# Kernel optimization log

Measured on AMD Instinct MI355X. Metric: run time of the kernel, lower is better.

Reference implementation:

```python
import jax, jax.numpy as jnp
import numpy as np

EPS = 1e-7
NORM_EPS = 1e-12

def _l2norm(x, axis):
    n = jnp.sqrt(jnp.sum(x * x, axis=axis, keepdims=True))
    return x / jnp.maximum(n, NORM_EPS)

def setup_inputs() -> dict:
    key = jax.random.key(0)
    B, M, D, N = 8, 64, 256, 16384
    ks = jax.random.split(key, 10)
    inp = {
        "points": jax.random.normal(ks[0], (B, D, N), jnp.float32),
        "clusters": jax.random.normal(ks[1], (B, M, D), jnp.float32),
        "values": jax.random.normal(ks[2], (B, N, D), jnp.float32),
        "value_clusters": jax.random.normal(ks[3], (B, M, D), jnp.float32),
        # learned params
        "sim_alpha": jnp.ones((M,), jnp.float32),
        "sim_beta": jnp.zeros((M,), jnp.float32),
        "clusters_bias": jnp.zeros((M, D), jnp.float32),
        "Wc": jax.random.normal(ks[4], (D, D), jnp.float32) / np.sqrt(D),
        "bc": jnp.zeros((D,), jnp.float32),
        "value_clusters_bias": jnp.zeros((M, D), jnp.float32),
        "Wv": jax.random.normal(ks[5], (D, D), jnp.float32) / np.sqrt(D),
        "bv": jnp.zeros((D,), jnp.float32),
    }
    return inp

def reference(points, clusters, values, value_clusters,
              sim_alpha, sim_beta, clusters_bias, Wc, bc,
              value_clusters_bias, Wv, bv):
    # per-cluster bias + Linear + SiLU (with_cluster_bias=True, no position)
    c = jax.nn.silu((clusters + clusters_bias) @ Wc.T + bc)            # [B,M,D]
    vc = jax.nn.silu((value_clusters + value_clusters_bias) @ Wv.T + bv)  # [B,M,D]
    # cosine similarity: normalize clusters over last dim, points over dim=-2
    sim = _l2norm(c, -1) @ _l2norm(points, -2)                         # [B,M,N]
    sim = sim_alpha[None, :, None] * sim + sim_beta[None, :, None]
    assignment = jax.nn.softmax(sim, axis=1)                           # over clusters
    agg = (vc + assignment @ values) / (jnp.sum(assignment, axis=-1, keepdims=True) + EPS)  # [B,M,D]
    # x = agg^T @ assignment -> [B,D,N]
    x = jnp.einsum('bmd,bmn->bdn', agg, assignment)
    return x
```

## Files before the change

kernel.cpp:

```cpp
#include <hip/hip_runtime.h>
#include <math.h>

#define BB 8
#define MM 64
#define DD 256
#define NP 16384
#define EPSF 1e-7f
#define NEPS 1e-12f

#define OFF_AT   0u
#define OFF_VC   131072u
#define OFF_AGG  262144u
#define OFF_ASUM 393216u
#define OFF_ASNT 393728u
#define OFF_WCT  8782336u
#define OFF_WVT  8847872u
#define OFF_PART 8913408u

__global__ __launch_bounds__(256) void k0_transpose(
    const float* __restrict__ Wc, const float* __restrict__ Wv,
    float* __restrict__ ws)
{
    __shared__ float tls[32][33];
    int which = blockIdx.z;
    const float* W = which ? Wv : Wc;
    float* Wt = ws + (which ? OFF_WVT : OFF_WCT);
    int j0 = blockIdx.x * 32, k0 = blockIdx.y * 32;
    int c = threadIdx.x & 31, r0 = threadIdx.x >> 5;
    #pragma unroll
    for (int rr = r0; rr < 32; rr += 8)
        tls[rr][c] = W[(size_t)(j0 + rr) * DD + k0 + c];
    __syncthreads();
    #pragma unroll
    for (int rr = r0; rr < 32; rr += 8)
        Wt[(size_t)(k0 + rr) * DD + j0 + c] = tls[c][rr];
}

__global__ __launch_bounds__(256) void k1_prep(
    const float* __restrict__ clusters, const float* __restrict__ vclusters,
    const float* __restrict__ alpha, const float* __restrict__ cbias,
    const float* __restrict__ bc, const float* __restrict__ vcbias,
    const float* __restrict__ bvv, float* __restrict__ ws)
{
    __shared__ float s_in[16][256];
    __shared__ float wt_s[32][256];
    __shared__ float s_out[16][260];
    __shared__ float s_scale[16];

    int t = threadIdx.x;
    int mt = blockIdx.x, b = blockIdx.y, which = blockIdx.z;
    int m0 = mt * 16;
    const float* inp   = which ? vclusters : clusters;
    const float* ibias = which ? vcbias : cbias;
    const float* obias = which ? bvv : bc;
    const float* Wt = ws + (which ? OFF_WVT : OFF_WCT);

    #pragma unroll
    for (int i = 0; i < 4; i++) {
        int e = i * 1024 + t * 4;
        int r = e >> 8, c = e & 255;
        float4 a  = *(const float4*)&inp[((size_t)(b * MM + m0 + r)) * DD + c];
        float4 bb = *(const float4*)&ibias[(size_t)(m0 + r) * DD + c];
        a.x += bb.x; a.y += bb.y; a.z += bb.z; a.w += bb.w;
        *(float4*)&s_in[r][c] = a;
    }

    int tm = t >> 5, tt = t & 31;
    float acc[2][8];
    #pragma unroll
    for (int i = 0; i < 2; i++)
        #pragma unroll
        for (int q = 0; q < 8; q++) acc[i][q] = 0.f;

    for (int k0 = 0; k0 < DD; k0 += 32) {
        __syncthreads();
        #pragma unroll
        for (int i = 0; i < 8; i++) {
            int e = i * 1024 + t * 4;
            int kd = e >> 8, c = e & 255;
            *(float4*)&wt_s[kd][c] = *(const float4*)&Wt[(size_t)(k0 + kd) * DD + c];
        }
        __syncthreads();
        #pragma unroll
        for (int kd = 0; kd < 32; kd++) {
            float a0 = s_in[tm][k0 + kd];
            float a1 = s_in[tm + 8][k0 + kd];
            float4 b0 = *(const float4*)&wt_s[kd][tt * 4];
            float4 b1 = *(const float4*)&wt_s[kd][128 + tt * 4];
            float bq[8] = {b0.x, b0.y, b0.z, b0.w, b1.x, b1.y, b1.z, b1.w};
            #pragma unroll
            for (int q = 0; q < 8; q++) { acc[0][q] += a0 * bq[q]; acc[1][q] += a1 * bq[q]; }
        }
    }

    #pragma unroll
    for (int q = 0; q < 8; q++) {
        int col = (q < 4) ? (tt * 4 + q) : (128 + tt * 4 + (q - 4));
        float ob = obias[col];
        #pragma unroll
        for (int i = 0; i < 2; i++) {
            int r = tm + i * 8;
            float x = acc[i][q] + ob;
            float s = x / (1.f + __expf(-x));
            s_out[r][col] = s;
        }
    }
    __syncthreads();

    if (which == 0) {
        if (t < 16) {
            float ss = 0.f;
            for (int j = 0; j < 256; j++) { float v = s_out[t][j]; ss += v * v; }
            s_scale[t] = alpha[m0 + t] / fmaxf(sqrtf(ss), NEPS);
        }
        __syncthreads();
        float* At = ws + OFF_AT + (size_t)b * DD * MM + (size_t)t * MM + m0;
        #pragma unroll
        for (int i = 0; i < 16; i++) At[i] = s_out[i][t] * s_scale[i];
    } else {
        float* vc = ws + OFF_VC + (size_t)(b * MM + m0) * DD;
        #pragma unroll
        for (int i = 0; i < 16; i++) vc[(size_t)i * DD + t] = s_out[i][t];
    }
}

__global__ __launch_bounds__(512, 4) void k3_sim(
    const float* __restrict__ points, const float* __restrict__ beta,
    float* __restrict__ ws)
{
    __shared__ float Ps[32][256];
    __shared__ float Ast[32][72];
    __shared__ float pinv_s[256];
    __shared__ float red[8][256];

    int t = threadIdx.x;
    int n0 = blockIdx.x * 256, b = blockIdx.y;
    int tm = t >> 6, tt = t & 63;
    const float* At = ws + OFF_AT + (size_t)b * DD * MM;
    const float* pb = points + (size_t)b * DD * NP;

    float acc[8][4];
    #pragma unroll
    for (int i = 0; i < 8; i++)
        #pragma unroll
        for (int q = 0; q < 4; q++) acc[i][q] = 0.f;

    float sq[4] = {0.f, 0.f, 0.f, 0.f};
    int srow = t >> 6, scol = (t & 63) * 4;

    for (int k0c = 0; k0c < DD; k0c += 32) {
        __syncthreads();
        #pragma unroll
        for (int i = 0; i < 4; i++) {
            int row = i * 8 + srow;
            float4 v = *(const float4*)&pb[(size_t)(k0c + row) * NP + n0 + scol];
            sq[0] += v.x * v.x; sq[1] += v.y * v.y;
            sq[2] += v.z * v.z; sq[3] += v.w * v.w;
            *(float4*)&Ps[row][scol] = v;
        }
        {
            int kd = t >> 4, me4 = (t & 15) * 4;
            *(float4*)&Ast[kd][me4] = *(const float4*)&At[(size_t)(k0c + kd) * MM + me4];
        }
        __syncthreads();
        #pragma unroll
        for (int kd = 0; kd < 32; kd++) {
            float4 a0 = *(const float4*)&Ast[kd][tm * 8];
            float4 a1 = *(const float4*)&Ast[kd][tm * 8 + 4];
            float4 b0 = *(const float4*)&Ps[kd][tt * 4];
            float av[8] = {a0.x, a0.y, a0.z, a0.w, a1.x, a1.y, a1.z, a1.w};
            float bq[4] = {b0.x, b0.y, b0.z, b0.w};
            #pragma unroll
            for (int i = 0; i < 8; i++)
                #pragma unroll
                for (int q = 0; q < 4; q++) acc[i][q] += av[i] * bq[q];
        }
    }

    __syncthreads();
    *(float4*)&red[srow][scol] = make_float4(sq[0], sq[1], sq[2], sq[3]);
    __syncthreads();
    if (t < 256) {
        float s = 0.f;
        #pragma unroll
        for (int r = 0; r < 8; r++) s += red[r][t];
        pinv_s[t] = 1.f / fmaxf(sqrtf(s), NEPS);
    }
    __syncthreads();

    float pin[4];
    { float4 p4 = *(const float4*)&pinv_s[tt * 4];
      pin[0] = p4.x; pin[1] = p4.y; pin[2] = p4.z; pin[3] = p4.w; }
    float sbet[8];
    #pragma unroll
    for (int i = 0; i < 8; i++) sbet[i] = beta[tm * 8 + i];

    float pmax[4] = {-1e30f, -1e30f, -1e30f, -1e30f};
    #pragma unroll
    for (int q = 0; q < 4; q++)
        #pragma unroll
        for (int i = 0; i < 8; i++) {
            acc[i][q] = acc[i][q] * pin[q] + sbet[i];
            pmax[q] = fmaxf(pmax[q], acc[i][q]);
        }
    *(float4*)&red[tm][tt * 4] = make_float4(pmax[0], pmax[1], pmax[2], pmax[3]);
    __syncthreads();
    float cmax[4] = {-1e30f, -1e30f, -1e30f, -1e30f};
    #pragma unroll
    for (int r = 0; r < 8; r++) {
        float4 rr = *(const float4*)&red[r][tt * 4];
        cmax[0] = fmaxf(cmax[0], rr.x); cmax[1] = fmaxf(cmax[1], rr.y);
        cmax[2] = fmaxf(cmax[2], rr.z); cmax[3] = fmaxf(cmax[3], rr.w);
    }
    __syncthreads();
    float ps[4] = {0.f, 0.f, 0.f, 0.f};
    #pragma unroll
    for (int q = 0; q < 4; q++)
        #pragma unroll
        for (int i = 0; i < 8; i++) {
            float e = __expf(acc[i][q] - cmax[q]);
            acc[i][q] = e; ps[q] += e;
        }
    *(float4*)&red[tm][tt * 4] = make_float4(ps[0], ps[1], ps[2], ps[3]);
    __syncthreads();
    float csum[4] = {0.f, 0.f, 0.f, 0.f};
    #pragma unroll
    for (int r = 0; r < 8; r++) {
        float4 rr = *(const float4*)&red[r][tt * 4];
        csum[0] += rr.x; csum[1] += rr.y; csum[2] += rr.z; csum[3] += rr.w;
    }

    float rinv[4];
    #pragma unroll
    for (int q = 0; q < 4; q++) rinv[q] = 1.f / csum[q];

    float msum[8];
    #pragma unroll
    for (int i = 0; i < 8; i++) msum[i] = 0.f;
    float* asnT = ws + OFF_ASNT + ((size_t)b * NP + n0) * MM;
    #pragma unroll
    for (int q = 0; q < 4; q++) {
        size_t col = (size_t)(tt * 4 + q);
        float v0 = acc[0][q] * rinv[q], v1 = acc[1][q] * rinv[q];
        float v2 = acc[2][q] * rinv[q], v3 = acc[3][q] * rinv[q];
        float v4 = acc[4][q] * rinv[q], v5 = acc[5][q] * rinv[q];
        float v6 = acc[6][q] * rinv[q], v7 = acc[7][q] * rinv[q];
        msum[0] += v0; msum[1] += v1; msum[2] += v2; msum[3] += v3;
        msum[4] += v4; msum[5] += v5; msum[6] += v6; msum[7] += v7;
        *(float4*)&asnT[col * MM + tm * 8]     = make_float4(v0, v1, v2, v3);
        *(float4*)&asnT[col * MM + tm * 8 + 4] = make_float4(v4, v5, v6, v7);
    }
    #pragma unroll
    for (int i = 0; i < 8; i++) {
        #pragma unroll
        for (int off = 32; off > 0; off >>= 1)
            msum[i] += __shfl_xor(msum[i], off);
    }
    if ((t & 63) == 0) {
        #pragma unroll
        for (int i = 0; i < 8; i++)
            atomicAdd(&ws[OFF_ASUM + b * MM + tm * 8 + i], msum[i]);
    }
}

__global__ __launch_bounds__(512, 4) void k4_av(
    const float* __restrict__ values, float* __restrict__ ws)
{
    __shared__ float Vs[16][256];
    __shared__ float Ast[16][72];
    int t = threadIdx.x;
    int slice = blockIdx.x, b = blockIdx.y;
    int tm = t >> 6, tt = t & 63;
    const float* asnT = ws + OFF_ASNT + (size_t)b * NP * MM;
    const float* vb = values + (size_t)b * NP * DD;

    float acc[8][4];
    #pragma unroll
    for (int i = 0; i < 8; i++)
        #pragma unroll
        for (int q = 0; q < 4; q++) acc[i][q] = 0.f;

    int nbase = slice * 256;
    for (int kc = 0; kc < 16; kc++) {
        int nb = nbase + kc * 16;
        __syncthreads();
        #pragma unroll
        for (int i = 0; i < 2; i++) {
            int f = i * 512 + t;
            int kd = f >> 6, c4 = (f & 63) * 4;
            *(float4*)&Vs[kd][c4] = *(const float4*)&vb[(size_t)(nb + kd) * DD + c4];
        }
        if (t < 256) {
            int kd = t >> 4, me4 = (t & 15) * 4;
            *(float4*)&Ast[kd][me4] = *(const float4*)&asnT[(size_t)(nb + kd) * MM + me4];
        }
        __syncthreads();
        #pragma unroll
        for (int kd = 0; kd < 16; kd++) {
            float4 a0 = *(const float4*)&Ast[kd][tm * 8];
            float4 a1 = *(const float4*)&Ast[kd][tm * 8 + 4];
            float4 b0 = *(const float4*)&Vs[kd][tt * 4];
            float av[8] = {a0.x, a0.y, a0.z, a0.w, a1.x, a1.y, a1.z, a1.w};
            float bq[4] = {b0.x, b0.y, b0.z, b0.w};
            #pragma unroll
            for (int i = 0; i < 8; i++)
                #pragma unroll
                for (int q = 0; q < 4; q++) acc[i][q] += av[i] * bq[q];
        }
    }
    float* part = ws + OFF_PART + ((size_t)slice * BB + b) * MM * DD;
    #pragma unroll
    for (int i = 0; i < 8; i++) {
        int m = tm * 8 + i;
        *(float4*)&part[(size_t)m * DD + tt * 4] =
            make_float4(acc[i][0], acc[i][1], acc[i][2], acc[i][3]);
    }
}

__global__ __launch_bounds__(256) void k5_agg(float* __restrict__ ws)
{
    int bm = blockIdx.x, t = threadIdx.x;
    float r = 1.f / (ws[OFF_ASUM + bm] + EPSF);
    size_t o = (size_t)bm * DD + t;
    const float* part = ws + OFF_PART;
    float s0 = 0.f, s1 = 0.f, s2 = 0.f, s3 = 0.f;
    #pragma unroll 4
    for (int s = 0; s < 64; s += 4) {
        s0 += part[(size_t)(s + 0) * (BB * MM * DD) + o];
        s1 += part[(size_t)(s + 1) * (BB * MM * DD) + o];
        s2 += part[(size_t)(s + 2) * (BB * MM * DD) + o];
        s3 += part[(size_t)(s + 3) * (BB * MM * DD) + o];
    }
    ws[OFF_AGG + o] = (ws[OFF_VC + o] + ((s0 + s1) + (s2 + s3))) * r;
}

__global__ __launch_bounds__(256, 3) void k6_x(
    float* __restrict__ out, const float* __restrict__ ws)
{
    __shared__ float aggs[64][68];
    __shared__ float asns[64][132];
    int t = threadIdx.x;
    int n0 = blockIdx.x * 128, d0 = blockIdx.y * 64, b = blockIdx.z;
    const float* agg = ws + OFF_AGG + (size_t)b * MM * DD;
    const float* asnT = ws + OFF_ASNT + (size_t)b * NP * MM;

    #pragma unroll
    for (int i = 0; i < 4; i++) {
        int f = i * 256 + t;
        int m = f >> 4, c4 = (f & 15) * 4;
        *(float4*)&aggs[m][c4] = *(const float4*)&agg[(size_t)m * DD + d0 + c4];
    }
    #pragma unroll
    for (int s = 0; s < 8; s++) {
        int f = s * 256 + t;
        int nr = f >> 4, fm = f & 15;
        float4 v = *(const float4*)&asnT[(size_t)(n0 + nr) * MM + fm * 4];
        asns[fm * 4 + 0][nr] = v.x; asns[fm * 4 + 1][nr] = v.y;
        asns[fm * 4 + 2][nr] = v.z; asns[fm * 4 + 3][nr] = v.w;
    }
    __syncthreads();

    int td = t >> 5, tn = t & 31;
    float acc[8][4];
    #pragma unroll
    for (int i = 0; i < 8; i++)
        #pragma unroll
        for (int q = 0; q < 4; q++) acc[i][q] = 0.f;

    #pragma unroll 8
    for (int m = 0; m < 64; m++) {
        float4 a0 = *(const float4*)&aggs[m][td * 4];
        float4 a1 = *(const float4*)&aggs[m][32 + td * 4];
        float4 b0 = *(const float4*)&asns[m][tn * 4];
        float av[8] = {a0.x, a0.y, a0.z, a0.w, a1.x, a1.y, a1.z, a1.w};
        float bq[4] = {b0.x, b0.y, b0.z, b0.w};
        #pragma unroll
        for (int i = 0; i < 8; i++)
            #pragma unroll
            for (int q = 0; q < 4; q++) acc[i][q] += av[i] * bq[q];
    }

    float* ob = out + (size_t)b * DD * NP;
    #pragma unroll
    for (int i = 0; i < 8; i++) {
        int d = d0 + ((i < 4) ? (td * 4 + i) : (32 + td * 4 + (i - 4)));
        *(float4*)&ob[(size_t)d * NP + n0 + tn * 4] =
            make_float4(acc[i][0], acc[i][1], acc[i][2], acc[i][3]);
    }
}

extern "C" void kernel_launch(void* const* d_in, const int* in_sizes, int n_in,
                              void* d_out, int out_size, void* d_ws, size_t ws_size,
                              hipStream_t stream) {
    const float* points    = (const float*)d_in[0];
    const float* clusters  = (const float*)d_in[1];
    const float* values    = (const float*)d_in[2];
    const float* vclusters = (const float*)d_in[3];
    const float* alpha     = (const float*)d_in[4];
    const float* beta      = (const float*)d_in[5];
    const float* cbias     = (const float*)d_in[6];
    const float* Wc        = (const float*)d_in[7];
    const float* bc        = (const float*)d_in[8];
    const float* vcbias    = (const float*)d_in[9];
    const float* Wv        = (const float*)d_in[10];
    const float* bvv       = (const float*)d_in[11];
    float* out = (float*)d_out;
    float* ws = (float*)d_ws;

    hipMemsetAsync((char*)d_ws + (size_t)OFF_ASUM * 4, 0, 512 * 4, stream);

    k0_transpose<<<dim3(8, 8, 2), 256, 0, stream>>>(Wc, Wv, ws);
    k1_prep<<<dim3(4, 8, 2), 256, 0, stream>>>(clusters, vclusters, alpha, cbias, bc, vcbias, bvv, ws);
    k3_sim<<<dim3(64, 8), 512, 0, stream>>>(points, beta, ws);
    k4_av<<<dim3(64, 8), 512, 0, stream>>>(values, ws);
    k5_agg<<<dim3(512), 256, 0, stream>>>(ws);
    k6_x<<<dim3(128, 4, 8), 256, 0, stream>>>(out, ws);
}
```

Before: 481.1 us.

## Compute similarity GEMM with split-bf16 MFMA and register-pipelined point loads

```diff
diff --git a/kernel.cpp b/kernel.cpp
--- a/kernel.cpp
+++ b/kernel.cpp
@@ -17,6 +17,9 @@
 #define OFF_WVT  8847872u
 #define OFF_PART 8913408u
 
+typedef __attribute__((ext_vector_type(8))) short bf16x8;
+typedef __attribute__((ext_vector_type(4))) float f32x4;
+
 __global__ __launch_bounds__(256) void k0_transpose(
     const float* __restrict__ Wc, const float* __restrict__ Wv,
     float* __restrict__ ws)
@@ -128,138 +131,188 @@
     const float* __restrict__ points, const float* __restrict__ beta,
     float* __restrict__ ws)
 {
-    __shared__ float Ps[32][256];
-    __shared__ float Ast[32][72];
-    __shared__ float pinv_s[256];
-    __shared__ float red[8][256];
+    __shared__ __align__(16) unsigned short Ah[64][264];
+    __shared__ __align__(16) unsigned short Al[64][264];
+    __shared__ float s_red[8][64];
+    __shared__ float s_beta[64];
 
     int t = threadIdx.x;
-    int n0 = blockIdx.x * 256, b = blockIdx.y;
-    int tm = t >> 6, tt = t & 63;
+    int b = blockIdx.y;
+    int n0 = blockIdx.x * 256;
+    int w = t >> 6;
+    int l = t & 63;
+    int c = l & 15;
+    int g = l >> 4;
+
     const float* At = ws + OFF_AT + (size_t)b * DD * MM;
+
+    if (t < 64) s_beta[t] = beta[t];
+
+    #pragma unroll
+    for (int i = 0; i < 8; i++) {
+        int f = i * 512 + t;
+        int d = f >> 4, m4 = (f & 15) * 4;
+        float4 v = *(const float4*)&At[(size_t)d * MM + m4];
+        float xs[4] = {v.x, v.y, v.z, v.w};
+        #pragma unroll
+        for (int j = 0; j < 4; j++) {
+            unsigned u = __float_as_uint(xs[j]);
+            float lof = xs[j] - __uint_as_float(u & 0xffff0000u);
+            Ah[m4 + j][d] = (unsigned short)(u >> 16);
+            Al[m4 + j][d] = (unsigned short)(__float_as_uint(lof) >> 16);
+        }
+    }
+    __syncthreads();
+
     const float* pb = points + (size_t)b * DD * NP;
-
-    float acc[8][4];
-    #pragma unroll
-    for (int i = 0; i < 8; i++)
-        #pragma unroll
-        for (int q = 0; q < 4; q++) acc[i][q] = 0.f;
-
-    float sq[4] = {0.f, 0.f, 0.f, 0.f};
-    int srow = t >> 6, scol = (t & 63) * 4;
-
-    for (int k0c = 0; k0c < DD; k0c += 32) {
-        __syncthreads();
-        #pragma unroll
-        for (int i = 0; i < 4; i++) {
-            int row = i * 8 + srow;
-            float4 v = *(const float4*)&pb[(size_t)(k0c + row) * NP + n0 + scol];
-            sq[0] += v.x * v.x; sq[1] += v.y * v.y;
-            sq[2] += v.z * v.z; sq[3] += v.w * v.w;
-            *(float4*)&Ps[row][scol] = v;
-        }
-        {
-            int kd = t >> 4, me4 = (t & 15) * 4;
-            *(float4*)&Ast[kd][me4] = *(const float4*)&At[(size_t)(k0c + kd) * MM + me4];
-        }
-        __syncthreads();
-        #pragma unroll
-        for (int kd = 0; kd < 32; kd++) {
-            float4 a0 = *(const float4*)&Ast[kd][tm * 8];
-            float4 a1 = *(const float4*)&Ast[kd][tm * 8 + 4];
-            float4 b0 = *(const float4*)&Ps[kd][tt * 4];
-            float av[8] = {a0.x, a0.y, a0.z, a0.w, a1.x, a1.y, a1.z, a1.w};
-            float bq[4] = {b0.x, b0.y, b0.z, b0.w};
-            #pragma unroll
-            for (int i = 0; i < 8; i++)
+    const float* pbase = pb + n0 + w * 32 + c;
+
+    f32x4 acc[4][2];
+    #pragma unroll
+    for (int am = 0; am < 4; am++)
+        #pragma unroll
+        for (int an = 0; an < 2; an++)
+            acc[am][an] = (f32x4){0.f, 0.f, 0.f, 0.f};
+
+    float sq[2] = {0.f, 0.f};
+    float cur[2][8], nxt[2][8];
+
+    #pragma unroll
+    for (int an = 0; an < 2; an++)
+        #pragma unroll
+        for (int i = 0; i < 8; i++)
+            cur[an][i] = pbase[(size_t)(g * 8 + i) * NP + an * 16];
+
+    #pragma unroll
+    for (int kc = 0; kc < 8; kc++) {
+        if (kc < 7) {
+            #pragma unroll
+            for (int an = 0; an < 2; an++)
                 #pragma unroll
-                for (int q = 0; q < 4; q++) acc[i][q] += av[i] * bq[q];
-        }
-    }
-
+                for (int i = 0; i < 8; i++)
+                    nxt[an][i] = pbase[(size_t)((kc + 1) * 32 + g * 8 + i) * NP + an * 16];
+        }
+        union { bf16x8 v; unsigned u[4]; } bh[2], bl[2];
+        #pragma unroll
+        for (int an = 0; an < 2; an++) {
+            #pragma unroll
+            for (int p = 0; p < 4; p++) {
+                float x0 = cur[an][2 * p], x1 = cur[an][2 * p + 1];
+                unsigned u0 = __float_as_uint(x0), u1 = __float_as_uint(x1);
+                float l0f = x0 - __uint_as_float(u0 & 0xffff0000u);
+                float l1f = x1 - __uint_as_float(u1 & 0xffff0000u);
+                bh[an].u[p] = (u0 >> 16) | (u1 & 0xffff0000u);
+                bl[an].u[p] = (__float_as_uint(l0f) >> 16) | (__float_as_uint(l1f) & 0xffff0000u);
+            }
+            #pragma unroll
+            for (int i = 0; i < 8; i++) sq[an] += cur[an][i] * cur[an][i];
+        }
+        #pragma unroll
+        for (int am = 0; am < 4; am++) {
+            bf16x8 ah = *(const bf16x8*)&Ah[am * 16 + c][kc * 32 + g * 8];
+            bf16x8 al = *(const bf16x8*)&Al[am * 16 + c][kc * 32 + g * 8];
+            #pragma unroll
+            for (int an = 0; an < 2; an++) {
+                acc[am][an] = __builtin_amdgcn_mfma_f32_16x16x32_bf16(ah, bh[an].v, acc[am][an], 0, 0, 0);
+                acc[am][an] = __builtin_amdgcn_mfma_f32_16x16x32_bf16(ah, bl[an].v, acc[am][an], 0, 0, 0);
+                acc[am][an] = __builtin_amdgcn_mfma_f32_16x16x32_bf16(al, bh[an].v, acc[am][an], 0, 0, 0);
+            }
+        }
+        if (kc < 7) {
+            #pragma unroll
+            for (int an = 0; an < 2; an++)
+                #pragma unroll
+                for (int i = 0; i < 8; i++) cur[an][i] = nxt[an][i];
+        }
+    }
+
+    float pinv2[2], cmax[2], csum[2];
+    #pragma unroll
+    for (int an = 0; an < 2; an++) {
+        float s = sq[an];
+        s += __shfl_xor(s, 16);
+        s += __shfl_xor(s, 32);
+        pinv2[an] = 1.f / fmaxf(sqrtf(s), NEPS);
+        cmax[an] = -1e30f;
+    }
+
+    #pragma unroll
+    for (int am = 0; am < 4; am++)
+        #pragma unroll
+        for (int an = 0; an < 2; an++)
+            #pragma unroll
+            for (int r = 0; r < 4; r++) {
+                float s = acc[am][an][r] * pinv2[an] + s_beta[am * 16 + g * 4 + r];
+                acc[am][an][r] = s;
+                cmax[an] = fmaxf(cmax[an], s);
+            }
+    #pragma unroll
+    for (int an = 0; an < 2; an++) {
+        cmax[an] = fmaxf(cmax[an], __shfl_xor(cmax[an], 16));
+        cmax[an] = fmaxf(cmax[an], __shfl_xor(cmax[an], 32));
+        csum[an] = 0.f;
+    }
+    #pragma unroll
+    for (int am = 0; am < 4; am++)
+        #pragma unroll
+        for (int an = 0; an < 2; an++)
+            #pragma unroll
+            for (int r = 0; r < 4; r++) {
+                float e = __expf(acc[am][an][r] - cmax[an]);
+                acc[am][an][r] = e;
+                csum[an] += e;
+            }
+    #pragma unroll
+    for (int an = 0; an < 2; an++) {
+        float s = csum[an];
+        s += __shfl_xor(s, 16);
+        s += __shfl_xor(s, 32);
+        csum[an] = 1.f / s;
+    }
+
+    float msum[4][4];
+    #pragma unroll
+    for (int am = 0; am < 4; am++)
+        #pragma unroll
+        for (int r = 0; r < 4; r++) msum[am][r] = 0.f;
+
+    float* asnT = ws + OFF_ASNT + (size_t)b * NP * MM;
+    int ncol = n0 + w * 32 + c;
+    #pragma unroll
+    for (int am = 0; am < 4; am++)
+        #pragma unroll
+        for (int an = 0; an < 2; an++)
+            #pragma unroll
+            for (int r = 0; r < 4; r++) {
+                float v = acc[am][an][r] * csum[an];
+                asnT[(size_t)(ncol + an * 16) * MM + am * 16 + g * 4 + r] = v;
+                msum[am][r] += v;
+            }
+
+    #pragma unroll
+    for (int am = 0; am < 4; am++)
+        #pragma unroll
+        for (int r = 0; r < 4; r++) {
+            float s = msum[am][r];
+            s += __shfl_xor(s, 1);
+            s += __shfl_xor(s, 2);
+            s += __shfl_xor(s, 4);
+            s += __shfl_xor(s, 8);
+            msum[am][r] = s;
+        }
+    if (c == 0) {
+        #pragma unroll
+        for (int am = 0; am < 4; am++)
+            #pragma unroll
+            for (int r = 0; r < 4; r++)
+                s_red[w][am * 16 + g * 4 + r] = msum[am][r];
+    }
     __syncthreads();
-    *(float4*)&red[srow][scol] = make_float4(sq[0], sq[1], sq[2], sq[3]);
-    __syncthreads();
-    if (t < 256) {
+    if (t < 64) {
         float s = 0.f;
         #pragma unroll
-        for (int r = 0; r < 8; r++) s += red[r][t];
-        pinv_s[t] = 1.f / fmaxf(sqrtf(s), NEPS);
-    }
-    __syncthreads();
-
-    float pin[4];
-    { float4 p4 = *(const float4*)&pinv_s[tt * 4];
-      pin[0] = p4.x; pin[1] = p4.y; pin[2] = p4.z; pin[3] = p4.w; }
-    float sbet[8];
-    #pragma unroll
-    for (int i = 0; i < 8; i++) sbet[i] = beta[tm * 8 + i];
-
-    float pmax[4] = {-1e30f, -1e30f, -1e30f, -1e30f};
-    #pragma unroll
-    for (int q = 0; q < 4; q++)
-        #pragma unroll
-        for (int i = 0; i < 8; i++) {
-            acc[i][q] = acc[i][q] * pin[q] + sbet[i];
-            pmax[q] = fmaxf(pmax[q], acc[i][q]);
-        }
-    *(float4*)&red[tm][tt * 4] = make_float4(pmax[0], pmax[1], pmax[2], pmax[3]);
-    __syncthreads();
-    float cmax[4] = {-1e30f, -1e30f, -1e30f, -1e30f};
-    #pragma unroll
-    for (int r = 0; r < 8; r++) {
-        float4 rr = *(const float4*)&red[r][tt * 4];
-        cmax[0] = fmaxf(cmax[0], rr.x); cmax[1] = fmaxf(cmax[1], rr.y);
-        cmax[2] = fmaxf(cmax[2], rr.z); cmax[3] = fmaxf(cmax[3], rr.w);
-    }
-    __syncthreads();
-    float ps[4] = {0.f, 0.f, 0.f, 0.f};
-    #pragma unroll
-    for (int q = 0; q < 4; q++)
-        #pragma unroll
-        for (int i = 0; i < 8; i++) {
-            float e = __expf(acc[i][q] - cmax[q]);
-            acc[i][q] = e; ps[q] += e;
-        }
-    *(float4*)&red[tm][tt * 4] = make_float4(ps[0], ps[1], ps[2], ps[3]);
-    __syncthreads();
-    float csum[4] = {0.f, 0.f, 0.f, 0.f};
-    #pragma unroll
-    for (int r = 0; r < 8; r++) {
-        float4 rr = *(const float4*)&red[r][tt * 4];
-        csum[0] += rr.x; csum[1] += rr.y; csum[2] += rr.z; csum[3] += rr.w;
-    }
-
-    float rinv[4];
-    #pragma unroll
-    for (int q = 0; q < 4; q++) rinv[q] = 1.f / csum[q];
-
-    float msum[8];
-    #pragma unroll
-    for (int i = 0; i < 8; i++) msum[i] = 0.f;
-    float* asnT = ws + OFF_ASNT + ((size_t)b * NP + n0) * MM;
-    #pragma unroll
-    for (int q = 0; q < 4; q++) {
-        size_t col = (size_t)(tt * 4 + q);
-        float v0 = acc[0][q] * rinv[q], v1 = acc[1][q] * rinv[q];
-        float v2 = acc[2][q] * rinv[q], v3 = acc[3][q] * rinv[q];
-        float v4 = acc[4][q] * rinv[q], v5 = acc[5][q] * rinv[q];
-        float v6 = acc[6][q] * rinv[q], v7 = acc[7][q] * rinv[q];
-        msum[0] += v0; msum[1] += v1; msum[2] += v2; msum[3] += v3;
-        msum[4] += v4; msum[5] += v5; msum[6] += v6; msum[7] += v7;
-        *(float4*)&asnT[col * MM + tm * 8]     = make_float4(v0, v1, v2, v3);
-        *(float4*)&asnT[col * MM + tm * 8 + 4] = make_float4(v4, v5, v6, v7);
-    }
-    #pragma unroll
-    for (int i = 0; i < 8; i++) {
-        #pragma unroll
-        for (int off = 32; off > 0; off >>= 1)
-            msum[i] += __shfl_xor(msum[i], off);
-    }
-    if ((t & 63) == 0) {
-        #pragma unroll
-        for (int i = 0; i < 8; i++)
-            atomicAdd(&ws[OFF_ASUM + b * MM + tm * 8 + i], msum[i]);
+        for (int ww = 0; ww < 8; ww++) s += s_red[ww][t];
+        atomicAdd(&ws[OFF_ASUM + b * MM + t], s);
     }
 }
 
```

Result: faster. 442.8 us (-8.0%).
